# Optimization experiments

Hardware: AMD Instinct MI355X
Metric: run time of the kernel (lower is better)

Reference implementation:

```python
import jax, jax.numpy as jnp
import numpy as np

B, C, H, W = 4, 48, 512, 512

def gaussian_kernel(kernel_size, channels):
    # matches torch get_gaussian_kernel: sigma from OpenCV rule
    sigma = 0.3 * ((kernel_size - 1) * 0.5 - 1) + 0.8
    grid = np.arange(kernel_size, dtype=np.float32) - kernel_size // 2
    k1 = np.exp(-grid ** 2 / (2 * sigma ** 2))
    k1 /= k1.sum()
    k2 = np.outer(k1, k1)  # [k,k]
    # OIHW depthwise: [C, 1, k, k]
    return jnp.asarray(np.broadcast_to(k2, (channels, 1, kernel_size, kernel_size)))

def depthwise_conv(x, kernel, pad):
    # x: [B,C,H,W], kernel: [C,1,k,k]
    return jax.lax.conv_general_dilated(
        x, kernel,
        window_strides=(1, 1),
        padding=((pad, pad), (pad, pad)),
        dimension_numbers=('NCHW', 'OIHW', 'NCHW'),
        feature_group_count=x.shape[1])

def setup_inputs() -> dict:
    key = jax.random.key(0)
    s = jax.random.normal(key, (B, C, H, W), dtype=jnp.float32)
    one = jnp.ones((), dtype=jnp.float32)
    return {'s': s, 'w1': one, 'w2': one, 'w3': one, 'w4': one}

def reference(s, w1, w2, w3, w4):
    channels = s.shape[1]
    k3 = gaussian_kernel(3, channels)
    k5 = gaussian_kernel(5, channels)
    k7 = gaussian_kernel(7, channels)
    s3 = depthwise_conv(s, k3, 1)
    s5 = depthwise_conv(s, k5, 2)
    s7 = depthwise_conv(s, k7, 3)
    # fused diff + weighted sum: w1*s + w2*(s-s3) + w3*(s3-s5) + w4*(s5-s7)
    return w1 * s + w2 * (s - s3) + w3 * (s3 - s5) + w4 * (s5 - s7)
```

## Files before the change

kernel.cpp:

```cpp
#include <hip/hip_runtime.h>
#include <math.h>

#define TX 64
#define TY 16
#define IN_W 72
#define IN_H 22

struct GaussCoefs {
    float g3[3];
    float g5[5];
    float g7[7];
};

__global__ __launch_bounds__(256) void mgdf_kernel(
    const float* __restrict__ s,
    const float* __restrict__ w1p, const float* __restrict__ w2p,
    const float* __restrict__ w3p, const float* __restrict__ w4p,
    float* __restrict__ out,
    GaussCoefs gc, int Wd, int Hd)
{
    __shared__ float in_tile[IN_H][IN_W];
    __shared__ float h3s[IN_H][TX];
    __shared__ float h5s[IN_H][TX];
    __shared__ float h7s[IN_H][TX];

    const int tid = threadIdx.x;
    const int plane = blockIdx.z;
    const int x0 = blockIdx.x * TX;
    const int y0 = blockIdx.y * TY;
    const float* sp = s + (size_t)plane * Hd * Wd;

    const float w1 = *w1p, w2 = *w2p, w3 = *w3p, w4 = *w4p;
    const float a0 = w1 + w2;
    const float a3 = w3 - w2;
    const float a5 = w4 - w3;
    const float a7 = -w4;

    for (int c = tid; c < (IN_W / 4) * IN_H; c += 256) {
        const int r  = c / (IN_W / 4);
        const int c4 = c % (IN_W / 4);
        const int gy = y0 - 3 + r;
        const int gx = x0 - 4 + c4 * 4;
        float4 v = make_float4(0.f, 0.f, 0.f, 0.f);
        if (gy >= 0 && gy < Hd) {
            const float* rowp = sp + (size_t)gy * Wd;
            if (gx >= 0 && gx + 3 < Wd) {
                v = *(const float4*)(rowp + gx);
            } else {
                float tmp[4];
                #pragma unroll
                for (int j = 0; j < 4; ++j) {
                    const int x = gx + j;
                    tmp[j] = (x >= 0 && x < Wd) ? rowp[x] : 0.f;
                }
                v = make_float4(tmp[0], tmp[1], tmp[2], tmp[3]);
            }
        }
        *(float4*)&in_tile[r][c4 * 4] = v;
    }
    __syncthreads();

    for (int task = tid; task < IN_H * (TX / 4); task += 256) {
        const int r  = task / (TX / 4);
        const int ch = task % (TX / 4);
        const float* row = &in_tile[r][ch * 4];
        const float4 va = *(const float4*)(row);
        const float4 vb = *(const float4*)(row + 4);
        const float4 vc = *(const float4*)(row + 8);
        const float v[12] = {va.x, va.y, va.z, va.w,
                             vb.x, vb.y, vb.z, vb.w,
                             vc.x, vc.y, vc.z, vc.w};
        float o3[4], o5[4], o7[4];
        #pragma unroll
        for (int j = 0; j < 4; ++j) {
            float h7 = 0.f;
            #pragma unroll
            for (int i = 0; i < 7; ++i) h7 = fmaf(gc.g7[i], v[j + 1 + i], h7);
            float h5 = 0.f;
            #pragma unroll
            for (int i = 0; i < 5; ++i) h5 = fmaf(gc.g5[i], v[j + 2 + i], h5);
            float h3 = 0.f;
            #pragma unroll
            for (int i = 0; i < 3; ++i) h3 = fmaf(gc.g3[i], v[j + 3 + i], h3);
            o3[j] = h3; o5[j] = h5; o7[j] = h7;
        }
        *(float4*)&h3s[r][ch * 4] = make_float4(o3[0], o3[1], o3[2], o3[3]);
        *(float4*)&h5s[r][ch * 4] = make_float4(o5[0], o5[1], o5[2], o5[3]);
        *(float4*)&h7s[r][ch * 4] = make_float4(o7[0], o7[1], o7[2], o7[3]);
    }
    __syncthreads();

    const int tx = tid & 15;
    const int ty = tid >> 4;
    const int xb = tx * 4;

    float acc3[4] = {0.f, 0.f, 0.f, 0.f};
    float acc5[4] = {0.f, 0.f, 0.f, 0.f};
    float acc7[4] = {0.f, 0.f, 0.f, 0.f};

    #pragma unroll
    for (int i = 0; i < 7; ++i) {
        const float4 hv = *(const float4*)&h7s[ty + i][xb];
        acc7[0] = fmaf(gc.g7[i], hv.x, acc7[0]);
        acc7[1] = fmaf(gc.g7[i], hv.y, acc7[1]);
        acc7[2] = fmaf(gc.g7[i], hv.z, acc7[2]);
        acc7[3] = fmaf(gc.g7[i], hv.w, acc7[3]);
    }
    #pragma unroll
    for (int i = 0; i < 5; ++i) {
        const float4 hv = *(const float4*)&h5s[ty + 1 + i][xb];
        acc5[0] = fmaf(gc.g5[i], hv.x, acc5[0]);
        acc5[1] = fmaf(gc.g5[i], hv.y, acc5[1]);
        acc5[2] = fmaf(gc.g5[i], hv.z, acc5[2]);
        acc5[3] = fmaf(gc.g5[i], hv.w, acc5[3]);
    }
    #pragma unroll
    for (int i = 0; i < 3; ++i) {
        const float4 hv = *(const float4*)&h3s[ty + 2 + i][xb];
        acc3[0] = fmaf(gc.g3[i], hv.x, acc3[0]);
        acc3[1] = fmaf(gc.g3[i], hv.y, acc3[1]);
        acc3[2] = fmaf(gc.g3[i], hv.z, acc3[2]);
        acc3[3] = fmaf(gc.g3[i], hv.w, acc3[3]);
    }

    const float4 sv = *(const float4*)&in_tile[ty + 3][xb + 4];
    float4 o;
    o.x = a0 * sv.x + a3 * acc3[0] + a5 * acc5[0] + a7 * acc7[0];
    o.y = a0 * sv.y + a3 * acc3[1] + a5 * acc5[1] + a7 * acc7[1];
    o.z = a0 * sv.z + a3 * acc3[2] + a5 * acc5[2] + a7 * acc7[2];
    o.w = a0 * sv.w + a3 * acc3[3] + a5 * acc5[3] + a7 * acc7[3];

    float* outp = out + (size_t)plane * Hd * Wd + (size_t)(y0 + ty) * Wd + x0 + xb;
    *(float4*)outp = o;
}

static void fill_gauss(float* g, int k) {
    const double sigma = 0.3 * ((k - 1) * 0.5 - 1.0) + 0.8;
    double t[7], sum = 0.0;
    for (int i = 0; i < k; ++i) {
        const double x = (double)(i - k / 2);
        t[i] = exp(-x * x / (2.0 * sigma * sigma));
        sum += t[i];
    }
    for (int i = 0; i < k; ++i) g[i] = (float)(t[i] / sum);
}

extern "C" void kernel_launch(void* const* d_in, const int* in_sizes, int n_in,
                              void* d_out, int out_size, void* d_ws, size_t ws_size,
                              hipStream_t stream) {
    const float* s  = (const float*)d_in[0];
    const float* w1 = (const float*)d_in[1];
    const float* w2 = (const float*)d_in[2];
    const float* w3 = (const float*)d_in[3];
    const float* w4 = (const float*)d_in[4];
    float* out = (float*)d_out;

    const int Hd = 512, Wd = 512;
    const int planes = in_sizes[0] / (Hd * Wd);

    GaussCoefs gc;
    fill_gauss(gc.g3, 3);
    fill_gauss(gc.g5, 5);
    fill_gauss(gc.g7, 7);

    dim3 grid(Wd / TX, Hd / TY, planes);
    mgdf_kernel<<<grid, 256, 0, stream>>>(s, w1, w2, w3, w4, out, gc, Wd, Hd);
}
```

Baseline: 371.1 us.

## Register-block vertical pass over larger tiles, dropping shared horizontal buffers

Tiles grow to 256x32, and each thread now computes an 8-row by 4-column strip. The horizontal convolution results stay in registers and are scattered straight into per-row accumulators, which removes the three shared-memory intermediate arrays and the second barrier. The output weights are folded into the vertical coefficients. This cuts halo overhead and shared-memory traffic but raises register pressure (32 accumulators plus temporaries) and reduces the number of blocks.

```diff
diff --git a/kernel.cpp b/kernel.cpp
--- a/kernel.cpp
+++ b/kernel.cpp
@@ -1,10 +1,11 @@
 #include <hip/hip_runtime.h>
 #include <math.h>
 
-#define TX 64
-#define TY 16
-#define IN_W 72
-#define IN_H 22
+#define TILE_X 256
+#define TILE_Y 32
+#define IN_W (TILE_X + 8)
+#define IN_H (TILE_Y + 6)
+#define NCHUNK (IN_W / 4)
 
 struct GaussCoefs {
     float g3[3];
@@ -12,23 +13,21 @@
     float g7[7];
 };
 
-__global__ __launch_bounds__(256) void mgdf_kernel(
+__global__ __launch_bounds__(256, 4) void mgdf_kernel(
     const float* __restrict__ s,
     const float* __restrict__ w1p, const float* __restrict__ w2p,
     const float* __restrict__ w3p, const float* __restrict__ w4p,
     float* __restrict__ out,
-    GaussCoefs gc, int Wd, int Hd)
+    GaussCoefs gc)
 {
     __shared__ float in_tile[IN_H][IN_W];
-    __shared__ float h3s[IN_H][TX];
-    __shared__ float h5s[IN_H][TX];
-    __shared__ float h7s[IN_H][TX];
 
     const int tid = threadIdx.x;
     const int plane = blockIdx.z;
-    const int x0 = blockIdx.x * TX;
-    const int y0 = blockIdx.y * TY;
-    const float* sp = s + (size_t)plane * Hd * Wd;
+    const int x0 = blockIdx.x * TILE_X;
+    const int y0 = blockIdx.y * TILE_Y;
+    const int Wd = 512, Hd = 512;
+    const float* sp = s + (size_t)plane * (Hd * Wd);
 
     const float w1 = *w1p, w2 = *w2p, w3 = *w3p, w4 = *w4p;
     const float a0 = w1 + w2;
@@ -36,9 +35,17 @@
     const float a5 = w4 - w3;
     const float a7 = -w4;
 
-    for (int c = tid; c < (IN_W / 4) * IN_H; c += 256) {
-        const int r  = c / (IN_W / 4);
-        const int c4 = c % (IN_W / 4);
+    float cv3[3], cv5[5], cv7[7];
+#pragma unroll
+    for (int t = 0; t < 3; ++t) cv3[t] = a3 * gc.g3[t];
+#pragma unroll
+    for (int t = 0; t < 5; ++t) cv5[t] = a5 * gc.g5[t];
+#pragma unroll
+    for (int t = 0; t < 7; ++t) cv7[t] = a7 * gc.g7[t];
+
+    for (int c = tid; c < IN_H * NCHUNK; c += 256) {
+        const int r  = c / NCHUNK;
+        const int c4 = c % NCHUNK;
         const int gy = y0 - 3 + r;
         const int gx = x0 - 4 + c4 * 4;
         float4 v = make_float4(0.f, 0.f, 0.f, 0.f);
@@ -48,7 +55,7 @@
                 v = *(const float4*)(rowp + gx);
             } else {
                 float tmp[4];
-                #pragma unroll
+#pragma unroll
                 for (int j = 0; j < 4; ++j) {
                     const int x = gx + j;
                     tmp[j] = (x >= 0 && x < Wd) ? rowp[x] : 0.f;
@@ -60,78 +67,83 @@
     }
     __syncthreads();
 
-    for (int task = tid; task < IN_H * (TX / 4); task += 256) {
-        const int r  = task / (TX / 4);
-        const int ch = task % (TX / 4);
-        const float* row = &in_tile[r][ch * 4];
-        const float4 va = *(const float4*)(row);
-        const float4 vb = *(const float4*)(row + 4);
-        const float4 vc = *(const float4*)(row + 8);
-        const float v[12] = {va.x, va.y, va.z, va.w,
-                             vb.x, vb.y, vb.z, vb.w,
-                             vc.x, vc.y, vc.z, vc.w};
-        float o3[4], o5[4], o7[4];
-        #pragma unroll
-        for (int j = 0; j < 4; ++j) {
-            float h7 = 0.f;
-            #pragma unroll
-            for (int i = 0; i < 7; ++i) h7 = fmaf(gc.g7[i], v[j + 1 + i], h7);
-            float h5 = 0.f;
-            #pragma unroll
-            for (int i = 0; i < 5; ++i) h5 = fmaf(gc.g5[i], v[j + 2 + i], h5);
-            float h3 = 0.f;
-            #pragma unroll
-            for (int i = 0; i < 3; ++i) h3 = fmaf(gc.g3[i], v[j + 3 + i], h3);
-            o3[j] = h3; o5[j] = h5; o7[j] = h7;
+    const int tx = tid & 63;
+    const int ystrip = tid >> 2;
+    const int ys = tid >> 6;
+    (void)ystrip;
+    const int xb = tx * 4;
+    const int row0 = ys * 8;
+
+    float acc[8][4];
+#pragma unroll
+    for (int j = 0; j < 8; ++j)
+#pragma unroll
+        for (int c = 0; c < 4; ++c) acc[j][c] = 0.f;
+
+#pragma unroll
+    for (int i = 0; i < 14; ++i) {
+        const float* rp = &in_tile[row0 + i][xb];
+        const float4 A = *(const float4*)(rp);
+        const float4 Bv = *(const float4*)(rp + 4);
+        const float4 Cv = *(const float4*)(rp + 8);
+        const float v[12] = {A.x, A.y, A.z, A.w,
+                             Bv.x, Bv.y, Bv.z, Bv.w,
+                             Cv.x, Cv.y, Cv.z, Cv.w};
+
+        float h7r[4], h5r[4], h3r[4];
+#pragma unroll
+        for (int c = 0; c < 4; ++c) {
+            float h = 0.f;
+#pragma unroll
+            for (int t = 0; t < 7; ++t) h = fmaf(gc.g7[t], v[c + 1 + t], h);
+            h7r[c] = h;
         }
-        *(float4*)&h3s[r][ch * 4] = make_float4(o3[0], o3[1], o3[2], o3[3]);
-        *(float4*)&h5s[r][ch * 4] = make_float4(o5[0], o5[1], o5[2], o5[3]);
-        *(float4*)&h7s[r][ch * 4] = make_float4(o7[0], o7[1], o7[2], o7[3]);
-    }
-    __syncthreads();
+        if (i >= 1 && i <= 12) {
+#pragma unroll
+            for (int c = 0; c < 4; ++c) {
+                float h = 0.f;
+#pragma unroll
+                for (int t = 0; t < 5; ++t) h = fmaf(gc.g5[t], v[c + 2 + t], h);
+                h5r[c] = h;
+            }
+        }
+        if (i >= 2 && i <= 11) {
+#pragma unroll
+            for (int c = 0; c < 4; ++c) {
+                float h = 0.f;
+#pragma unroll
+                for (int t = 0; t < 3; ++t) h = fmaf(gc.g3[t], v[c + 3 + t], h);
+                h3r[c] = h;
+            }
+        }
 
-    const int tx = tid & 15;
-    const int ty = tid >> 4;
-    const int xb = tx * 4;
-
-    float acc3[4] = {0.f, 0.f, 0.f, 0.f};
-    float acc5[4] = {0.f, 0.f, 0.f, 0.f};
-    float acc7[4] = {0.f, 0.f, 0.f, 0.f};
-
-    #pragma unroll
-    for (int i = 0; i < 7; ++i) {
-        const float4 hv = *(const float4*)&h7s[ty + i][xb];
-        acc7[0] = fmaf(gc.g7[i], hv.x, acc7[0]);
-        acc7[1] = fmaf(gc.g7[i], hv.y, acc7[1]);
-        acc7[2] = fmaf(gc.g7[i], hv.z, acc7[2]);
-        acc7[3] = fmaf(gc.g7[i], hv.w, acc7[3]);
-    }
-    #pragma unroll
-    for (int i = 0; i < 5; ++i) {
-        const float4 hv = *(const float4*)&h5s[ty + 1 + i][xb];
-        acc5[0] = fmaf(gc.g5[i], hv.x, acc5[0]);
-        acc5[1] = fmaf(gc.g5[i], hv.y, acc5[1]);
-        acc5[2] = fmaf(gc.g5[i], hv.z, acc5[2]);
-        acc5[3] = fmaf(gc.g5[i], hv.w, acc5[3]);
-    }
-    #pragma unroll
-    for (int i = 0; i < 3; ++i) {
-        const float4 hv = *(const float4*)&h3s[ty + 2 + i][xb];
-        acc3[0] = fmaf(gc.g3[i], hv.x, acc3[0]);
-        acc3[1] = fmaf(gc.g3[i], hv.y, acc3[1]);
-        acc3[2] = fmaf(gc.g3[i], hv.z, acc3[2]);
-        acc3[3] = fmaf(gc.g3[i], hv.w, acc3[3]);
+#pragma unroll
+        for (int d = 0; d < 7; ++d) {
+            const int j = i - d;
+            if (j < 0 || j > 7) continue;
+#pragma unroll
+            for (int c = 0; c < 4; ++c) {
+                float t = acc[j][c];
+                t = fmaf(cv7[d], h7r[c], t);
+                if (d >= 1 && d <= 5) t = fmaf(cv5[d - 1], h5r[c], t);
+                if (d >= 2 && d <= 4) t = fmaf(cv3[d - 2], h3r[c], t);
+                acc[j][c] = t;
+            }
+        }
+        if (i >= 3 && i <= 10) {
+            const int j = i - 3;
+#pragma unroll
+            for (int c = 0; c < 4; ++c)
+                acc[j][c] = fmaf(a0, v[4 + c], acc[j][c]);
+        }
     }
 
-    const float4 sv = *(const float4*)&in_tile[ty + 3][xb + 4];
-    float4 o;
-    o.x = a0 * sv.x + a3 * acc3[0] + a5 * acc5[0] + a7 * acc7[0];
-    o.y = a0 * sv.y + a3 * acc3[1] + a5 * acc5[1] + a7 * acc7[1];
-    o.z = a0 * sv.z + a3 * acc3[2] + a5 * acc5[2] + a7 * acc7[2];
-    o.w = a0 * sv.w + a3 * acc3[3] + a5 * acc5[3] + a7 * acc7[3];
-
-    float* outp = out + (size_t)plane * Hd * Wd + (size_t)(y0 + ty) * Wd + x0 + xb;
-    *(float4*)outp = o;
+    float* outp = out + (size_t)plane * (Hd * Wd) + (size_t)(y0 + row0) * Wd + x0 + xb;
+#pragma unroll
+    for (int j = 0; j < 8; ++j) {
+        *(float4*)(outp + (size_t)j * Wd) =
+            make_float4(acc[j][0], acc[j][1], acc[j][2], acc[j][3]);
+    }
 }
 
 static void fill_gauss(float* g, int k) {
@@ -163,6 +175,6 @@
     fill_gauss(gc.g5, 5);
     fill_gauss(gc.g7, 7);
 
-    dim3 grid(Wd / TX, Hd / TY, planes);
-    mgdf_kernel<<<grid, 256, 0, stream>>>(s, w1, w2, w3, w4, out, gc, Wd, Hd);
+    dim3 grid(Wd / TILE_X, Hd / TILE_Y, planes);
+    mgdf_kernel<<<grid, 256, 0, stream>>>(s, w1, w2, w3, w4, out, gc);
 }
```

After: 495.7 us. 33.6% more time.
